# Performance work log

Hardware: AMD Instinct MI355X
Metric: run time of the kernel (lower is better)

Reference implementation:

```python
import jax, jax.numpy as jnp
import numpy as np

# Standard HBV parameter bounds (lo, hi), order matches theta columns 0..12
BOUNDS = [
    ("parBETA",   1.0,   6.0),
    ("parFC",    50.0, 1000.0),
    ("parK0",     0.05,  0.9),
    ("parK1",     0.01,  0.5),
    ("parK2",     0.001, 0.2),
    ("parLP",     0.2,   1.0),
    ("parPERC",   0.0,  10.0),
    ("parUZL",    0.0, 100.0),
    ("parTT",    -2.5,   2.5),
    ("parCFMAX",  0.5,  10.0),
    ("parCFR",    0.0,   0.1),
    ("parCWH",    0.0,   0.2),
    ("parBETAET", 0.3,   5.0),
]


def setup_inputs() -> dict:
    key = jax.random.key(0)
    k1, k2, k3 = jax.random.split(key, 3)
    B, T = 100000, 365
    y = jax.random.uniform(k1, (B, 5), dtype=jnp.float32) * 100.0          # states (mm)
    theta = jax.random.uniform(k2, (B, 13), dtype=jnp.float32)             # normalized params in [0,1]
    clim = jax.random.uniform(k3, (T, B, 3), dtype=jnp.float32)
    # columns: P in [0,20] mm/d, T in [-10,25] C, Ep in [0,6] mm/d
    scale = jnp.array([20.0, 35.0, 6.0], dtype=jnp.float32)
    shift = jnp.array([0.0, -10.0, 0.0], dtype=jnp.float32)
    climate_data = clim * scale + shift
    return {"y": y, "theta": theta, "climate_data": climate_data, "t": 100}


def reference(y, theta, climate_data, t):
    # Denormalize parameters
    pars = {}
    for i, (name, lo, hi) in enumerate(BOUNDS):
        pars[name] = lo + theta[:, i] * (hi - lo)
    Beta, FC = pars["parBETA"], pars["parFC"]
    K0, K1, K2 = pars["parK0"], pars["parK1"], pars["parK2"]
    LP, PERC, UZL = pars["parLP"], pars["parPERC"], pars["parUZL"]
    TT, CFMAX, CFR = pars["parTT"], pars["parCFMAX"], pars["parCFR"]
    CWH, BETAET = pars["parCWH"], pars["parBETAET"]

    SNOWPACK = jnp.clip(y[:, 0], 0.0, None)
    MELTWATER = jnp.clip(y[:, 1], 0.0, None)
    SM = jnp.clip(y[:, 2], 1e-8, None)
    SUZ = jnp.clip(y[:, 3], 0.0, None)
    SLZ = jnp.clip(y[:, 4], 0.0, None)

    climate_in = climate_data[t]           # [B, 3]
    P, T_, Ep = climate_in[:, 0], climate_in[:, 1], climate_in[:, 2]

    # fluxes
    flux_sf = jnp.where(T_ < TT, P, 0.0)                                   # snowfall
    flux_refr = jnp.minimum(jnp.clip(CFR * CFMAX * (TT - T_), 0.0, None), MELTWATER)
    flux_melt = jnp.minimum(jnp.clip(CFMAX * (T_ - TT), 0.0, None), SNOWPACK)
    flux_rf = jnp.where(T_ >= TT, P, 0.0)                                  # rainfall
    flux_Isnow = jnp.clip(MELTWATER - CWH * SNOWPACK, 0.0, None)           # to-soil
    soil_wetness = jnp.clip((SM / FC) ** Beta, 0.0, 1.0)
    flux_PEFF = (flux_rf + flux_Isnow) * soil_wetness
    flux_ex = jnp.clip(SM - FC, 0.0, None)
    evapfactor = jnp.clip((SM / (LP * FC)) ** BETAET, 0.0, 1.0)
    flux_et = jnp.minimum(SM, Ep * evapfactor)
    flux_perc = jnp.minimum(SUZ, PERC)
    flux_q0 = K0 * jnp.clip(SUZ - UZL, 0.0, None)
    flux_q1 = K1 * SUZ
    flux_q2 = K2 * SLZ

    dS = jnp.stack([
        flux_sf + flux_refr - flux_melt,
        flux_melt - flux_refr - flux_Isnow,
        flux_Isnow + flux_rf - flux_PEFF - flux_ex - flux_et,
        flux_PEFF + flux_ex - flux_perc - flux_q0 - flux_q1,
        flux_perc - flux_q2,
    ], axis=1)                                                             # [B, 5]
    fluxes = (flux_q0 + flux_q1 + flux_q2)[:, None]                        # [B, 1]
    return dS, fluxes
```

## Files before the change

kernel.cpp:

```cpp
#include <hip/hip_runtime.h>


__global__ __launch_bounds__(256) void hbv_step_kernel(
    const float* __restrict__ y,
    const float* __restrict__ theta,
    const float* __restrict__ clim,
    const int* __restrict__ tptr,
    float* __restrict__ out,
    int B)
{
    const int b = blockIdx.x * blockDim.x + threadIdx.x;
    if (b >= B) return;

    const int t = tptr[0];

    const float* yr = y + (size_t)b * 5;
    const float* th = theta + (size_t)b * 13;
    const float* cr = clim + ((size_t)t * (size_t)B + (size_t)b) * 3;

    const float parBETA   = 1.0f   + th[0]  * (6.0f   - 1.0f);
    const float parFC     = 50.0f  + th[1]  * (1000.0f- 50.0f);
    const float parK0     = 0.05f  + th[2]  * (0.9f   - 0.05f);
    const float parK1     = 0.01f  + th[3]  * (0.5f   - 0.01f);
    const float parK2     = 0.001f + th[4]  * (0.2f   - 0.001f);
    const float parLP     = 0.2f   + th[5]  * (1.0f   - 0.2f);
    const float parPERC   = 0.0f   + th[6]  * (10.0f  - 0.0f);
    const float parUZL    = 0.0f   + th[7]  * (100.0f - 0.0f);
    const float parTT     = -2.5f  + th[8]  * (2.5f   - (-2.5f));
    const float parCFMAX  = 0.5f   + th[9]  * (10.0f  - 0.5f);
    const float parCFR    = 0.0f   + th[10] * (0.1f   - 0.0f);
    const float parCWH    = 0.0f   + th[11] * (0.2f   - 0.0f);
    const float parBETAET = 0.3f   + th[12] * (5.0f   - 0.3f);

    const float SNOWPACK  = fmaxf(yr[0], 0.0f);
    const float MELTWATER = fmaxf(yr[1], 0.0f);
    const float SM        = fmaxf(yr[2], 1e-8f);
    const float SUZ       = fmaxf(yr[3], 0.0f);
    const float SLZ       = fmaxf(yr[4], 0.0f);

    const float P  = cr[0];
    const float T_ = cr[1];
    const float Ep = cr[2];

    const float flux_sf    = (T_ < parTT) ? P : 0.0f;
    const float flux_refr  = fminf(fmaxf(parCFR * parCFMAX * (parTT - T_), 0.0f), MELTWATER);
    const float flux_melt  = fminf(fmaxf(parCFMAX * (T_ - parTT), 0.0f), SNOWPACK);
    const float flux_rf    = (T_ >= parTT) ? P : 0.0f;
    const float flux_Isnow = fmaxf(MELTWATER - parCWH * SNOWPACK, 0.0f);

    const float soil_wetness = fminf(fmaxf(powf(SM / parFC, parBETA), 0.0f), 1.0f);
    const float flux_PEFF  = (flux_rf + flux_Isnow) * soil_wetness;
    const float flux_ex    = fmaxf(SM - parFC, 0.0f);
    const float evapfactor = fminf(fmaxf(powf(SM / (parLP * parFC), parBETAET), 0.0f), 1.0f);
    const float flux_et    = fminf(SM, Ep * evapfactor);

    const float flux_perc  = fminf(SUZ, parPERC);
    const float flux_q0    = parK0 * fmaxf(SUZ - parUZL, 0.0f);
    const float flux_q1    = parK1 * SUZ;
    const float flux_q2    = parK2 * SLZ;

    float* dS = out + (size_t)b * 5;
    dS[0] = flux_sf + flux_refr - flux_melt;
    dS[1] = flux_melt - flux_refr - flux_Isnow;
    dS[2] = flux_Isnow + flux_rf - flux_PEFF - flux_ex - flux_et;
    dS[3] = flux_PEFF + flux_ex - flux_perc - flux_q0 - flux_q1;
    dS[4] = flux_perc - flux_q2;
    out[(size_t)B * 5 + b] = flux_q0 + flux_q1 + flux_q2;
}

extern "C" void kernel_launch(void* const* d_in, const int* in_sizes, int n_in,
                              void* d_out, int out_size, void* d_ws, size_t ws_size,
                              hipStream_t stream) {
    const float* y     = (const float*)d_in[0];
    const float* theta = (const float*)d_in[1];
    const float* clim  = (const float*)d_in[2];
    const int*   tptr  = (const int*)d_in[3];
    float* out = (float*)d_out;

    const int B = in_sizes[0] / 5;

    const int block = 256;
    const int grid = (B + block - 1) / block;
    hbv_step_kernel<<<grid, block, 0, stream>>>(y, theta, clim, tptr, out, B);
}
```

Baseline: 9.611 us.

## Stage AoS rows through shared memory with coalesced float4 loads and stores

Each block cooperatively loads its y, theta and climate rows into LDS, using float4 vector loads for y and theta, then computes from LDS. Results are staged in LDS and written back with coalesced float4 stores. This removes the strided per-thread access to the 5/13/3-float rows. It also swaps powf for the faster, less accurate __powf and drops the redundant lower clamp. In exchange it adds about 27 KB of LDS per block and two barriers, which may reduce occupancy.

Result: slower. 9.855 us (+2.5%).

```diff
diff --git a/kernel.cpp b/kernel.cpp
--- a/kernel.cpp
+++ b/kernel.cpp
@@ -1,7 +1,9 @@
 #include <hip/hip_runtime.h>
 
 
-__global__ __launch_bounds__(256) void hbv_step_kernel(
+#define TPB 256
+
+__global__ __launch_bounds__(TPB) void hbv_step_kernel(
     const float* __restrict__ y,
     const float* __restrict__ theta,
     const float* __restrict__ clim,
@@ -9,63 +11,103 @@
     float* __restrict__ out,
     int B)
 {
-    const int b = blockIdx.x * blockDim.x + threadIdx.x;
-    if (b >= B) return;
+    __shared__ float sy [TPB * 5];
+    __shared__ float sth[TPB * 13];
+    __shared__ float sc [TPB * 3];
+    __shared__ float sdS[TPB * 5];
+    __shared__ float sfx[TPB];
 
-    const int t = tptr[0];
+    const int tid = threadIdx.x;
+    const int blk = blockIdx.x;
+    const int b0  = blk * TPB;
+    const int nb  = min(TPB, B - b0);
+    const int t   = tptr[0];
+    const size_t cbase = ((size_t)t * (size_t)B + (size_t)b0) * 3;
 
-    const float* yr = y + (size_t)b * 5;
-    const float* th = theta + (size_t)b * 13;
-    const float* cr = clim + ((size_t)t * (size_t)B + (size_t)b) * 3;
+    if (nb == TPB) {
+        const float4* y4  = (const float4*)y     + (size_t)blk * (TPB * 5 / 4);
+        const float4* th4 = (const float4*)theta + (size_t)blk * (TPB * 13 / 4);
+        float4* sy4  = (float4*)sy;
+        float4* sth4 = (float4*)sth;
+        #pragma unroll
+        for (int i = tid; i < TPB * 5 / 4; i += TPB)  sy4[i]  = y4[i];
+        #pragma unroll
+        for (int i = tid; i < TPB * 13 / 4; i += TPB) sth4[i] = th4[i];
+        #pragma unroll
+        for (int i = tid; i < TPB * 3; i += TPB)      sc[i]   = clim[cbase + i];
+    } else {
+        for (int i = tid; i < nb * 5; i += TPB)  sy[i]  = y[(size_t)b0 * 5 + i];
+        for (int i = tid; i < nb * 13; i += TPB) sth[i] = theta[(size_t)b0 * 13 + i];
+        for (int i = tid; i < nb * 3; i += TPB)  sc[i]  = clim[cbase + i];
+    }
+    __syncthreads();
 
-    const float parBETA   = 1.0f   + th[0]  * (6.0f   - 1.0f);
-    const float parFC     = 50.0f  + th[1]  * (1000.0f- 50.0f);
-    const float parK0     = 0.05f  + th[2]  * (0.9f   - 0.05f);
-    const float parK1     = 0.01f  + th[3]  * (0.5f   - 0.01f);
-    const float parK2     = 0.001f + th[4]  * (0.2f   - 0.001f);
-    const float parLP     = 0.2f   + th[5]  * (1.0f   - 0.2f);
-    const float parPERC   = 0.0f   + th[6]  * (10.0f  - 0.0f);
-    const float parUZL    = 0.0f   + th[7]  * (100.0f - 0.0f);
-    const float parTT     = -2.5f  + th[8]  * (2.5f   - (-2.5f));
-    const float parCFMAX  = 0.5f   + th[9]  * (10.0f  - 0.5f);
-    const float parCFR    = 0.0f   + th[10] * (0.1f   - 0.0f);
-    const float parCWH    = 0.0f   + th[11] * (0.2f   - 0.0f);
-    const float parBETAET = 0.3f   + th[12] * (5.0f   - 0.3f);
+    if (tid < nb) {
+        const float* th = sth + tid * 13;
+        const float* yr = sy + tid * 5;
+        const float* cr = sc + tid * 3;
 
-    const float SNOWPACK  = fmaxf(yr[0], 0.0f);
-    const float MELTWATER = fmaxf(yr[1], 0.0f);
-    const float SM        = fmaxf(yr[2], 1e-8f);
-    const float SUZ       = fmaxf(yr[3], 0.0f);
-    const float SLZ       = fmaxf(yr[4], 0.0f);
+        const float parBETA   = 1.0f   + th[0]  * 5.0f;
+        const float parFC     = 50.0f  + th[1]  * 950.0f;
+        const float parK0     = 0.05f  + th[2]  * 0.85f;
+        const float parK1     = 0.01f  + th[3]  * 0.49f;
+        const float parK2     = 0.001f + th[4]  * 0.199f;
+        const float parLP     = 0.2f   + th[5]  * 0.8f;
+        const float parPERC   =          th[6]  * 10.0f;
+        const float parUZL    =          th[7]  * 100.0f;
+        const float parTT     = -2.5f  + th[8]  * 5.0f;
+        const float parCFMAX  = 0.5f   + th[9]  * 9.5f;
+        const float parCFR    =          th[10] * 0.1f;
+        const float parCWH    =          th[11] * 0.2f;
+        const float parBETAET = 0.3f   + th[12] * 4.7f;
 
-    const float P  = cr[0];
-    const float T_ = cr[1];
-    const float Ep = cr[2];
+        const float SNOWPACK  = fmaxf(yr[0], 0.0f);
+        const float MELTWATER = fmaxf(yr[1], 0.0f);
+        const float SM        = fmaxf(yr[2], 1e-8f);
+        const float SUZ       = fmaxf(yr[3], 0.0f);
+        const float SLZ       = fmaxf(yr[4], 0.0f);
 
-    const float flux_sf    = (T_ < parTT) ? P : 0.0f;
-    const float flux_refr  = fminf(fmaxf(parCFR * parCFMAX * (parTT - T_), 0.0f), MELTWATER);
-    const float flux_melt  = fminf(fmaxf(parCFMAX * (T_ - parTT), 0.0f), SNOWPACK);
-    const float flux_rf    = (T_ >= parTT) ? P : 0.0f;
-    const float flux_Isnow = fmaxf(MELTWATER - parCWH * SNOWPACK, 0.0f);
+        const float P  = cr[0];
+        const float T_ = cr[1];
+        const float Ep = cr[2];
 
-    const float soil_wetness = fminf(fmaxf(powf(SM / parFC, parBETA), 0.0f), 1.0f);
-    const float flux_PEFF  = (flux_rf + flux_Isnow) * soil_wetness;
-    const float flux_ex    = fmaxf(SM - parFC, 0.0f);
-    const float evapfactor = fminf(fmaxf(powf(SM / (parLP * parFC), parBETAET), 0.0f), 1.0f);
-    const float flux_et    = fminf(SM, Ep * evapfactor);
+        const float flux_sf    = (T_ < parTT) ? P : 0.0f;
+        const float flux_refr  = fminf(fmaxf(parCFR * parCFMAX * (parTT - T_), 0.0f), MELTWATER);
+        const float flux_melt  = fminf(fmaxf(parCFMAX * (T_ - parTT), 0.0f), SNOWPACK);
+        const float flux_rf    = (T_ >= parTT) ? P : 0.0f;
+        const float flux_Isnow = fmaxf(MELTWATER - parCWH * SNOWPACK, 0.0f);
 
-    const float flux_perc  = fminf(SUZ, parPERC);
-    const float flux_q0    = parK0 * fmaxf(SUZ - parUZL, 0.0f);
-    const float flux_q1    = parK1 * SUZ;
-    const float flux_q2    = parK2 * SLZ;
+        const float soil_wetness = fminf(__powf(SM / parFC, parBETA), 1.0f);
+        const float flux_PEFF  = (flux_rf + flux_Isnow) * soil_wetness;
+        const float flux_ex    = fmaxf(SM - parFC, 0.0f);
+        const float evapfactor = fminf(__powf(SM / (parLP * parFC), parBETAET), 1.0f);
+        const float flux_et    = fminf(SM, Ep * evapfactor);
 
-    float* dS = out + (size_t)b * 5;
-    dS[0] = flux_sf + flux_refr - flux_melt;
-    dS[1] = flux_melt - flux_refr - flux_Isnow;
-    dS[2] = flux_Isnow + flux_rf - flux_PEFF - flux_ex - flux_et;
-    dS[3] = flux_PEFF + flux_ex - flux_perc - flux_q0 - flux_q1;
-    dS[4] = flux_perc - flux_q2;
-    out[(size_t)B * 5 + b] = flux_q0 + flux_q1 + flux_q2;
+        const float flux_perc  = fminf(SUZ, parPERC);
+        const float flux_q0    = parK0 * fmaxf(SUZ - parUZL, 0.0f);
+        const float flux_q1    = parK1 * SUZ;
+        const float flux_q2    = parK2 * SLZ;
+
+        float* d = sdS + tid * 5;
+        d[0] = flux_sf + flux_refr - flux_melt;
+        d[1] = flux_melt - flux_refr - flux_Isnow;
+        d[2] = flux_Isnow + flux_rf - flux_PEFF - flux_ex - flux_et;
+        d[3] = flux_PEFF + flux_ex - flux_perc - flux_q0 - flux_q1;
+        d[4] = flux_perc - flux_q2;
+        sfx[tid] = flux_q0 + flux_q1 + flux_q2;
+    }
+    __syncthreads();
+
+    if (nb == TPB) {
+        float4* o4 = (float4*)out + (size_t)blk * (TPB * 5 / 4);
+        const float4* s4 = (const float4*)sdS;
+        #pragma unroll
+        for (int i = tid; i < TPB * 5 / 4; i += TPB) o4[i] = s4[i];
+        out[(size_t)B * 5 + b0 + tid] = sfx[tid];
+    } else {
+        for (int i = tid; i < nb * 5; i += TPB) out[(size_t)b0 * 5 + i] = sdS[i];
+        if (tid < nb) out[(size_t)B * 5 + b0 + tid] = sfx[tid];
+    }
 }
 
 extern "C" void kernel_launch(void* const* d_in, const int* in_sizes, int n_in,
@@ -79,7 +121,6 @@
 
     const int B = in_sizes[0] / 5;
 
-    const int block = 256;
-    const int grid = (B + block - 1) / block;
-    hbv_step_kernel<<<grid, block, 0, stream>>>(y, theta, clim, tptr, out, B);
+    const int grid = (B + TPB - 1) / TPB;
+    hbv_step_kernel<<<grid, TPB, 0, stream>>>(y, theta, clim, tptr, out, B);
 }
```
